# Performance work log

Hardware: AMD Instinct MI355X
Metric: run time of the kernel (lower is better)

## Reference

```python
import jax, jax.numpy as jnp
import numpy as np

# Build the three 3x3x3 Sobel kernels once, stacked as [O=3, I=1, 3,3,3]
def _sobel_kernels():
    kx = np.array([[[-1,0,1],[-2,0,2],[-1,0,1]],
                   [[-2,0,2],[-4,0,4],[-2,0,2]],
                   [[-1,0,1],[-2,0,2],[-1,0,1]]], dtype=np.float32)
    ky = np.array([[[-1,-2,-1],[0,0,0],[1,2,1]],
                   [[-2,-4,-2],[0,0,0],[2,4,2]],
                   [[-1,-2,-1],[0,0,0],[1,2,1]]], dtype=np.float32)
    kz = np.array([[[-1,-2,-1],[-2,-4,-2],[-1,-2,-1]],
                   [[0,0,0],[0,0,0],[0,0,0]],
                   [[1,2,1],[2,4,2],[1,2,1]]], dtype=np.float32)
    return jnp.asarray(np.stack([kx, ky, kz])[:, None])  # [3,1,3,3,3]

_K = _sobel_kernels()
_EPS = 1e-08

def _grad_mag(x):
    # x: [B,1,D,H,W] -> fused conv producing all 3 gradient channels at once
    g = jax.lax.conv_general_dilated(
        x, _K, window_strides=(1, 1, 1), padding='SAME',
        dimension_numbers=('NCDHW', 'OIDHW', 'NCDHW'))  # [B,3,D,H,W]
    return jnp.sqrt(jnp.sum(g * g, axis=1, keepdims=True) + _EPS)  # [B,1,D,H,W]


def setup_inputs() -> dict:
    key = jax.random.key(0)
    k1, k2 = jax.random.split(key)
    shape = (2, 1, 160, 192, 160)
    pred = jax.random.normal(k1, shape, dtype=jnp.float32)
    target = jax.random.normal(k2, shape, dtype=jnp.float32)
    return {"pred": pred, "target": target}


def reference(pred, target):
    pg = _grad_mag(pred)
    tg = _grad_mag(target)
    # penalty='l1' -> F.l1_loss mean reduction
    return jnp.mean(jnp.abs(pg - tg))
```

## Files before the change

kernel.cpp:

```cpp
#include <hip/hip_runtime.h>

namespace {
constexpr int Wd = 160, Hd = 192, Dd = 160, Bd = 2;
constexpr int HW = Hd * Wd;
constexpr int THREADS = 256;
constexpr int ROWS_OUT = 6;
constexpr int ROWS_LDS = 8;
constexpr int RS = 164;
constexpr int STRIPS = 40;
constexpr int CTHREADS = ROWS_OUT * STRIPS;
constexpr int TASKS = 2 * ROWS_LDS * STRIPS;
constexpr int DCHUNK = 10;
constexpr int NCHUNK = Dd / DCHUNK;
constexpr int RGROUPS = Hd / ROWS_OUT;
constexpr float EPS = 1e-8f;
}

using v4f = __attribute__((ext_vector_type(4))) float;

__device__ __forceinline__ float dpp_up1(float v) {
  return __int_as_float(__builtin_amdgcn_update_dpp(
      0, __float_as_int(v), 0x138, 0xF, 0xF, true));
}
__device__ __forceinline__ float dpp_dn1(float v) {
  return __int_as_float(__builtin_amdgcn_update_dpp(
      0, __float_as_int(v), 0x130, 0xF, 0xF, true));
}

__global__ __launch_bounds__(THREADS) void sobel_loss_kernel(
    const float* __restrict__ pred, const float* __restrict__ targ,
    float* __restrict__ out) {
  __shared__ float lsw[2][ROWS_LDS][RS];
  __shared__ float ldw[2][ROWS_LDS][RS];
  const int tid = threadIdx.x;
  const int lane = tid & 63;
  const int h0 = blockIdx.x * ROWS_OUT;
  const int d0 = blockIdx.y * DCHUNK;
  const size_t volOff = (size_t)blockIdx.z * Dd * HW;
  const float* pb = pred + volOff;
  const float* tb = targ + volOff;

  const float* gs[3];
  float* psw[3];
  float* pdw[3];
  bool sok[3], rok[3], zL[3], zR[3], pL[3], pR[3];
#pragma unroll
  for (int u = 0; u < 3; ++u) {
    const int i = tid + 256 * u;
    const bool ok = (i < TASKS);
    const int ic = ok ? i : 0;
    const int t_ = ic / (ROWS_LDS * STRIPS);
    const int rem = ic - t_ * (ROWS_LDS * STRIPS);
    const int r8 = rem / STRIPS, s = rem - r8 * STRIPS;
    const int hh = h0 - 1 + r8;
    const bool rv = ok && ((unsigned)hh < (unsigned)Hd);
    sok[u] = ok;
    rok[u] = rv;
    zL[u] = (s == 0);
    zR[u] = (s == STRIPS - 1);
    pL[u] = ok && (lane == 0) && (s != 0);
    pR[u] = ok && (lane == 63) && (s != STRIPS - 1);
    gs[u] = (t_ ? tb : pb) + (size_t)(rv ? hh : 0) * Wd + s * 4;
    psw[u] = &lsw[t_][r8][s * 4];
    pdw[u] = &ldw[t_][r8][s * 4];
  }

  float4 m[3];
  float hl[3], hr[3];
  auto GLOAD = [&](int d) {
    const bool dok = (unsigned)d < (unsigned)Dd;
    const size_t so = (size_t)d * HW;
#pragma unroll
    for (int u = 0; u < 3; ++u) {
      float4 v = make_float4(0.f, 0.f, 0.f, 0.f);
      float a = 0.f, b = 0.f;
      if (dok && rok[u]) {
        v = *reinterpret_cast<const float4*>(gs[u] + so);
        if (pL[u]) a = gs[u][so - 1];
        if (pR[u]) b = gs[u][so + 4];
      }
      m[u] = v; hl[u] = a; hr[u] = b;
    }
  };

  auto STAGE = [&]() {
#pragma unroll
    for (int u = 0; u < 3; ++u) {
      float xl = dpp_up1(m[u].w);
      float xr = dpp_dn1(m[u].x);
      if (zL[u]) xl = 0.f;
      if (pL[u]) xl = hl[u];
      if (zR[u]) xr = 0.f;
      if (pR[u]) xr = hr[u];
      const float x0 = xl, x1 = m[u].x, x2 = m[u].y, x3 = m[u].z,
                  x4 = m[u].w, x5 = xr;
      float4 swv, dwv;
      swv.x = fmaf(2.f, x1, x0 + x2);  dwv.x = x2 - x0;
      swv.y = fmaf(2.f, x2, x1 + x3);  dwv.y = x3 - x1;
      swv.z = fmaf(2.f, x3, x2 + x4);  dwv.z = x4 - x2;
      swv.w = fmaf(2.f, x4, x3 + x5);  dwv.w = x5 - x3;
      if (sok[u]) {
        *reinterpret_cast<float4*>(psw[u]) = swv;
        *reinterpret_cast<float4*>(pdw[u]) = dwv;
      }
    }
  };

  const int cr = tid / STRIPS;
  const int cs4 = (tid - cr * STRIPS) * 4;
  const bool is_c = (tid < CTHREADS);

  v4f A[3][2], B[3][2], C[3][2];

  auto HCONV = [&](int slot) {
#pragma unroll
    for (int t_ = 0; t_ < 2; ++t_) {
      const v4f sm = *reinterpret_cast<const v4f*>(&lsw[t_][cr][cs4]);
      const v4f s0 = *reinterpret_cast<const v4f*>(&lsw[t_][cr + 1][cs4]);
      const v4f sp = *reinterpret_cast<const v4f*>(&lsw[t_][cr + 2][cs4]);
      const v4f dm = *reinterpret_cast<const v4f*>(&ldw[t_][cr][cs4]);
      const v4f dd = *reinterpret_cast<const v4f*>(&ldw[t_][cr + 1][cs4]);
      const v4f dp = *reinterpret_cast<const v4f*>(&ldw[t_][cr + 2][cs4]);
      A[slot][t_] = s0 * 2.f + (sm + sp);
      B[slot][t_] = dd * 2.f + (dm + dp);
      C[slot][t_] = sp - sm;
    }
  };

  v4f accv = {0.f, 0.f, 0.f, 0.f};

  GLOAD(d0 - 1);
  STAGE(); GLOAD(d0); __syncthreads();
  if (is_c) HCONV(0);
  __syncthreads();
  STAGE(); GLOAD(d0 + 1); __syncthreads();
  if (is_c) HCONV(1);
  __syncthreads();

#pragma unroll
  for (int k = 0; k < DCHUNK; ++k) {
    STAGE();
    if (k < DCHUNK - 1) GLOAD(d0 + 2 + k);
    __syncthreads();
    const int i0 = k % 3, i1 = (k + 1) % 3, i2 = (k + 2) % 3;
    if (is_c) {
      HCONV(i2);
      const v4f gx0 = B[i1][0] * 2.f + (B[i0][0] + B[i2][0]);
      const v4f gy0 = C[i1][0] * 2.f + (C[i0][0] + C[i2][0]);
      const v4f gz0 = A[i2][0] - A[i0][0];
      const v4f q0 = gx0 * gx0 + gy0 * gy0 + gz0 * gz0 + EPS;
      const v4f gx1 = B[i1][1] * 2.f + (B[i0][1] + B[i2][1]);
      const v4f gy1 = C[i1][1] * 2.f + (C[i0][1] + C[i2][1]);
      const v4f gz1 = A[i2][1] - A[i0][1];
      const v4f q1 = gx1 * gx1 + gy1 * gy1 + gz1 * gz1 + EPS;
      v4f dd_;
#pragma unroll
      for (int j = 0; j < 4; ++j)
        dd_[j] = __builtin_amdgcn_sqrtf(q0[j]) - __builtin_amdgcn_sqrtf(q1[j]);
#pragma unroll
      for (int j = 0; j < 4; ++j) dd_[j] = fabsf(dd_[j]);
      accv += dd_;
    }
    __syncthreads();
  }

  float sred = accv.x + accv.y + accv.z + accv.w;
#pragma unroll
  for (int off = 32; off > 0; off >>= 1) sred += __shfl_down(sred, off, 64);
  __shared__ float wsum[THREADS / 64];
  const int wid = tid >> 6;
  if (lane == 0) wsum[wid] = sred;
  __syncthreads();
  if (tid == 0) {
    float t = 0.f;
#pragma unroll
    for (int i = 0; i < THREADS / 64; ++i) t += wsum[i];
    atomicAdd(out, t * (1.0f / (float)((size_t)Bd * Dd * Hd * Wd)));
  }
}

extern "C" void kernel_launch(void* const* d_in, const int* in_sizes, int n_in,
                              void* d_out, int out_size, void* d_ws, size_t ws_size,
                              hipStream_t stream) {
  const float* pred = (const float*)d_in[0];
  const float* targ = (const float*)d_in[1];
  float* out = (float*)d_out;
  (void)in_sizes; (void)n_in; (void)out_size; (void)d_ws; (void)ws_size;

  hipMemsetAsync(out, 0, sizeof(float), stream);
  dim3 grid(RGROUPS, NCHUNK, Bd);
  sobel_loss_kernel<<<grid, THREADS, 0, stream>>>(pred, targ, out);
}
```

Before: 38.44 us.

## Warp-specialize Sobel kernel into producer and consumer warps with double-buffered LDS

Splits the 384-thread block into 128 producer threads, which load global planes and write the horizontal Sobel partials into LDS, and 256 consumer threads, which do the vertical and depth convolution plus the loss. The LDS staging buffer is double-buffered, so producers fill the next slab while consumers read the current one, cutting the two barriers per depth step to one. The aim is to overlap global loads and staging with the consumer math. In exchange each producer now handles 5 tasks serially instead of 3, the block uses more threads and twice the LDS, and 16 of the consumer threads sit idle.

```diff
diff --git a/kernel.cpp b/kernel.cpp
--- a/kernel.cpp
+++ b/kernel.cpp
@@ -3,13 +3,16 @@
 namespace {
 constexpr int Wd = 160, Hd = 192, Dd = 160, Bd = 2;
 constexpr int HW = Hd * Wd;
-constexpr int THREADS = 256;
+constexpr int THREADS = 384;
+constexpr int PTHREADS = 128;
 constexpr int ROWS_OUT = 6;
 constexpr int ROWS_LDS = 8;
 constexpr int RS = 164;
 constexpr int STRIPS = 40;
-constexpr int CTHREADS = ROWS_OUT * STRIPS;
+constexpr int COUTS = ROWS_OUT * STRIPS;
 constexpr int TASKS = 2 * ROWS_LDS * STRIPS;
+constexpr int PTASKS = TASKS / PTHREADS;
+constexpr int BUFSTRIDE = 2 * ROWS_LDS * RS;
 constexpr int DCHUNK = 10;
 constexpr int NCHUNK = Dd / DCHUNK;
 constexpr int RGROUPS = Hd / ROWS_OUT;
@@ -30,48 +33,47 @@
 __global__ __launch_bounds__(THREADS) void sobel_loss_kernel(
     const float* __restrict__ pred, const float* __restrict__ targ,
     float* __restrict__ out) {
-  __shared__ float lsw[2][ROWS_LDS][RS];
-  __shared__ float ldw[2][ROWS_LDS][RS];
+  __shared__ float lsw[2][2][ROWS_LDS][RS];
+  __shared__ float ldw[2][2][ROWS_LDS][RS];
   const int tid = threadIdx.x;
   const int lane = tid & 63;
+  const bool is_p = (tid < PTHREADS);
   const int h0 = blockIdx.x * ROWS_OUT;
   const int d0 = blockIdx.y * DCHUNK;
   const size_t volOff = (size_t)blockIdx.z * Dd * HW;
   const float* pb = pred + volOff;
   const float* tb = targ + volOff;
 
-  const float* gs[3];
-  float* psw[3];
-  float* pdw[3];
-  bool sok[3], rok[3], zL[3], zR[3], pL[3], pR[3];
+  const float* gs[PTASKS];
+  float* psw[PTASKS];
+  float* pdw[PTASKS];
+  bool rok[PTASKS], zL[PTASKS], zR[PTASKS], pL[PTASKS], pR[PTASKS];
+  float4 m[PTASKS];
+  float hl[PTASKS], hr[PTASKS];
+  if (is_p) {
 #pragma unroll
-  for (int u = 0; u < 3; ++u) {
-    const int i = tid + 256 * u;
-    const bool ok = (i < TASKS);
-    const int ic = ok ? i : 0;
-    const int t_ = ic / (ROWS_LDS * STRIPS);
-    const int rem = ic - t_ * (ROWS_LDS * STRIPS);
-    const int r8 = rem / STRIPS, s = rem - r8 * STRIPS;
-    const int hh = h0 - 1 + r8;
-    const bool rv = ok && ((unsigned)hh < (unsigned)Hd);
-    sok[u] = ok;
-    rok[u] = rv;
-    zL[u] = (s == 0);
-    zR[u] = (s == STRIPS - 1);
-    pL[u] = ok && (lane == 0) && (s != 0);
-    pR[u] = ok && (lane == 63) && (s != STRIPS - 1);
-    gs[u] = (t_ ? tb : pb) + (size_t)(rv ? hh : 0) * Wd + s * 4;
-    psw[u] = &lsw[t_][r8][s * 4];
-    pdw[u] = &ldw[t_][r8][s * 4];
+    for (int u = 0; u < PTASKS; ++u) {
+      const int i = tid + PTHREADS * u;
+      const int t_ = i / (ROWS_LDS * STRIPS);
+      const int rem = i - t_ * (ROWS_LDS * STRIPS);
+      const int r8 = rem / STRIPS, s = rem - r8 * STRIPS;
+      const int hh = h0 - 1 + r8;
+      rok[u] = ((unsigned)hh < (unsigned)Hd);
+      zL[u] = (s == 0);
+      zR[u] = (s == STRIPS - 1);
+      pL[u] = (lane == 0) && (s != 0);
+      pR[u] = (lane == 63) && (s != STRIPS - 1);
+      gs[u] = (t_ ? tb : pb) + (size_t)(rok[u] ? hh : 0) * Wd + s * 4;
+      psw[u] = &lsw[0][t_][r8][s * 4];
+      pdw[u] = &ldw[0][t_][r8][s * 4];
+    }
   }
 
-  float4 m[3];
-  float hl[3], hr[3];
   auto GLOAD = [&](int d) {
     const bool dok = (unsigned)d < (unsigned)Dd;
     const size_t so = (size_t)d * HW;
 #pragma unroll
-    for (int u = 0; u < 3; ++u) {
+    for (int u = 0; u < PTASKS; ++u) {
       float4 v = make_float4(0.f, 0.f, 0.f, 0.f);
       float a = 0.f, b = 0.f;
       if (dok && rok[u]) {
@@ -83,9 +85,9 @@
     }
   };
 
-  auto STAGE = [&]() {
+  auto STAGE = [&](int b) {
 #pragma unroll
-    for (int u = 0; u < 3; ++u) {
+    for (int u = 0; u < PTASKS; ++u) {
       float xl = dpp_up1(m[u].w);
       float xr = dpp_dn1(m[u].x);
       if (zL[u]) xl = 0.f;
@@ -99,28 +101,27 @@
       swv.y = fmaf(2.f, x2, x1 + x3);  dwv.y = x3 - x1;
       swv.z = fmaf(2.f, x3, x2 + x4);  dwv.z = x4 - x2;
       swv.w = fmaf(2.f, x4, x3 + x5);  dwv.w = x5 - x3;
-      if (sok[u]) {
-        *reinterpret_cast<float4*>(psw[u]) = swv;
-        *reinterpret_cast<float4*>(pdw[u]) = dwv;
-      }
+      *reinterpret_cast<float4*>(psw[u] + b * BUFSTRIDE) = swv;
+      *reinterpret_cast<float4*>(pdw[u] + b * BUFSTRIDE) = dwv;
     }
   };
 
-  const int cr = tid / STRIPS;
-  const int cs4 = (tid - cr * STRIPS) * 4;
-  const bool is_c = (tid < CTHREADS);
+  const int ctid = tid - PTHREADS;
+  const int cr = ctid / STRIPS;
+  const int cs4 = (ctid - cr * STRIPS) * 4;
+  const bool is_c = (!is_p) && (ctid < COUTS);
 
   v4f A[3][2], B[3][2], C[3][2];
 
-  auto HCONV = [&](int slot) {
+  auto HCONV = [&](int slot, int b) {
 #pragma unroll
     for (int t_ = 0; t_ < 2; ++t_) {
-      const v4f sm = *reinterpret_cast<const v4f*>(&lsw[t_][cr][cs4]);
-      const v4f s0 = *reinterpret_cast<const v4f*>(&lsw[t_][cr + 1][cs4]);
-      const v4f sp = *reinterpret_cast<const v4f*>(&lsw[t_][cr + 2][cs4]);
-      const v4f dm = *reinterpret_cast<const v4f*>(&ldw[t_][cr][cs4]);
-      const v4f dd = *reinterpret_cast<const v4f*>(&ldw[t_][cr + 1][cs4]);
-      const v4f dp = *reinterpret_cast<const v4f*>(&ldw[t_][cr + 2][cs4]);
+      const v4f sm = *reinterpret_cast<const v4f*>(&lsw[b][t_][cr][cs4]);
+      const v4f s0 = *reinterpret_cast<const v4f*>(&lsw[b][t_][cr + 1][cs4]);
+      const v4f sp = *reinterpret_cast<const v4f*>(&lsw[b][t_][cr + 2][cs4]);
+      const v4f dm = *reinterpret_cast<const v4f*>(&ldw[b][t_][cr][cs4]);
+      const v4f dd = *reinterpret_cast<const v4f*>(&ldw[b][t_][cr + 1][cs4]);
+      const v4f dp = *reinterpret_cast<const v4f*>(&ldw[b][t_][cr + 2][cs4]);
       A[slot][t_] = s0 * 2.f + (sm + sp);
       B[slot][t_] = dd * 2.f + (dm + dp);
       C[slot][t_] = sp - sm;
@@ -129,37 +130,40 @@
 
   v4f accv = {0.f, 0.f, 0.f, 0.f};
 
-  GLOAD(d0 - 1);
-  STAGE(); GLOAD(d0); __syncthreads();
-  if (is_c) HCONV(0);
-  __syncthreads();
-  STAGE(); GLOAD(d0 + 1); __syncthreads();
-  if (is_c) HCONV(1);
+  if (is_p) {
+    GLOAD(d0 - 1);
+    STAGE(0);
+    GLOAD(d0);
+  }
   __syncthreads();
 
 #pragma unroll
-  for (int k = 0; k < DCHUNK; ++k) {
-    STAGE();
-    if (k < DCHUNK - 1) GLOAD(d0 + 2 + k);
-    __syncthreads();
-    const int i0 = k % 3, i1 = (k + 1) % 3, i2 = (k + 2) % 3;
+  for (int j = 0; j < DCHUNK + 2; ++j) {
+    if (is_p) {
+      if (j < DCHUNK + 1) STAGE((j + 1) & 1);
+      if (j < DCHUNK) GLOAD(d0 + 1 + j);
+    }
     if (is_c) {
-      HCONV(i2);
-      const v4f gx0 = B[i1][0] * 2.f + (B[i0][0] + B[i2][0]);
-      const v4f gy0 = C[i1][0] * 2.f + (C[i0][0] + C[i2][0]);
-      const v4f gz0 = A[i2][0] - A[i0][0];
-      const v4f q0 = gx0 * gx0 + gy0 * gy0 + gz0 * gz0 + EPS;
-      const v4f gx1 = B[i1][1] * 2.f + (B[i0][1] + B[i2][1]);
-      const v4f gy1 = C[i1][1] * 2.f + (C[i0][1] + C[i2][1]);
-      const v4f gz1 = A[i2][1] - A[i0][1];
-      const v4f q1 = gx1 * gx1 + gy1 * gy1 + gz1 * gz1 + EPS;
-      v4f dd_;
+      HCONV(j % 3, j & 1);
+      if (j >= 2) {
+        const int i0 = (j + 1) % 3, i1 = (j + 2) % 3, i2 = j % 3;
+        const v4f gx0 = B[i1][0] * 2.f + (B[i0][0] + B[i2][0]);
+        const v4f gy0 = C[i1][0] * 2.f + (C[i0][0] + C[i2][0]);
+        const v4f gz0 = A[i2][0] - A[i0][0];
+        const v4f q0 = gx0 * gx0 + gy0 * gy0 + gz0 * gz0 + EPS;
+        const v4f gx1 = B[i1][1] * 2.f + (B[i0][1] + B[i2][1]);
+        const v4f gy1 = C[i1][1] * 2.f + (C[i0][1] + C[i2][1]);
+        const v4f gz1 = A[i2][1] - A[i0][1];
+        const v4f q1 = gx1 * gx1 + gy1 * gy1 + gz1 * gz1 + EPS;
+        v4f dd_;
 #pragma unroll
-      for (int j = 0; j < 4; ++j)
-        dd_[j] = __builtin_amdgcn_sqrtf(q0[j]) - __builtin_amdgcn_sqrtf(q1[j]);
+        for (int jj = 0; jj < 4; ++jj)
+          dd_[jj] = __builtin_amdgcn_sqrtf(q0[jj]) -
+                    __builtin_amdgcn_sqrtf(q1[jj]);
 #pragma unroll
-      for (int j = 0; j < 4; ++j) dd_[j] = fabsf(dd_[j]);
-      accv += dd_;
+        for (int jj = 0; jj < 4; ++jj) dd_[jj] = fabsf(dd_[jj]);
+        accv += dd_;
+      }
     }
     __syncthreads();
   }
```

Result: slower. 96.24 us (+150.4%).
